# Performance work log

Measured on AMD Instinct MI355X. Metric: run time of the kernel, lower is better.

The kernel has to match this reference:

```python
import jax, jax.numpy as jnp
import numpy as np

GAMMA = 1.0
BIG = 1e30  # finite stand-in for +inf to keep gradients NaN-free


def pairwise_sqdist(x, y):
    # x: [B, C, N], y: [B, C, M] -> [B, N, M] squared euclidean distances
    xx = jnp.sum(x * x, axis=1)                      # [B, N]
    yy = jnp.sum(y * y, axis=1)                      # [B, M]
    xy = jnp.einsum('bcn,bcm->bnm', x, y)            # [B, N, M]
    return xx[:, :, None] + yy[:, None, :] - 2.0 * xy


def soft_dtw(D, gamma):
    # Anti-diagonal wavefront soft-DTW DP.
    # R[i, j] = D[i-1, j-1] + softmin(R[i-1,j-1], R[i-1,j], R[i,j-1])
    # Diagonal d = i + j; store diag as [B, N+1] arrays indexed by i.
    B, N, M = D.shape
    i_idx = jnp.arange(N + 1)
    # d = 0 diagonal: R[0,0] = 0, everything else +inf
    diag0 = jnp.full((B, N + 1), BIG, D.dtype).at[:, 0].set(0.0)
    # d = 1 diagonal: R[1,0] and R[0,1] are +inf
    diag1 = jnp.full((B, N + 1), BIG, D.dtype)

    def step(carry, d):
        prev2, prev1 = carry                      # diagonals d-2, d-1
        j = d - i_idx                             # 1-based column index
        valid = (i_idx >= 1) & (i_idx <= N) & (j >= 1) & (j <= M)
        di = jnp.clip(i_idx - 1, 0, N - 1)
        dj = jnp.clip(j - 1, 0, M - 1)
        dvals = D[:, di, dj]                      # [B, N+1]
        r0 = jnp.roll(prev2, 1, axis=1)           # R[i-1, j-1]
        r1 = jnp.roll(prev1, 1, axis=1)           # R[i-1, j]
        r2 = prev1                                # R[i, j-1]
        stacked = jnp.stack([r0, r1, r2], axis=0)  # [3, B, N+1]
        softmin = -gamma * jax.nn.logsumexp(-stacked / gamma, axis=0)
        cur = jnp.where(valid[None, :], dvals + softmin, BIG)
        return (prev1, cur), None

    ds = jnp.arange(2, N + M + 1)
    (_, last), _ = jax.lax.scan(step, (diag0, diag1), ds)
    return last[:, N]                             # R[N, M] per batch


def setup_inputs() -> dict:
    key = jax.random.key(0)
    kx, ky = jax.random.split(key)
    B, C, N = 32, 80, 512
    x = jax.random.normal(kx, (B, C, N), dtype=jnp.float32)
    y = jax.random.normal(ky, (B, C, N), dtype=jnp.float32)
    return {"x": x, "y": y}


def reference(x, y):
    D = pairwise_sqdist(x, y)     # save_memory=True path
    return soft_dtw(D, GAMMA)     # [B], normalize=False; squeeze(0) is a no-op
```

## Files before the change

kernel.cpp:

```cpp
#include <hip/hip_runtime.h>
#include <hip/hip_bf16.h>

#define BIGF 1e30f
#define TC 80
#define TN 512
#define L2E 1.4426950408889634f
#define LN2 0.6931471805599453f

typedef float f32x2 __attribute__((ext_vector_type(2)));
typedef float f32x4 __attribute__((ext_vector_type(4)));
typedef short s16x8 __attribute__((ext_vector_type(8)));
typedef __attribute__((address_space(1))) const unsigned int gu32;
typedef __attribute__((address_space(3))) unsigned int lu32;

__global__ __launch_bounds__(256) void pairdist_kernel(
    const float* __restrict__ x, const float* __restrict__ y,
    float* __restrict__ F) {
  const int b  = blockIdx.z;
  const int n0 = blockIdx.x * 128;
  const int m0 = blockIdx.y * 128;

  __shared__ __align__(16) short Ab[128 * 128];
  __shared__ __align__(16) short Bb[128 * 128];
  __shared__ float xxs[128], yys[128];

  const float* xb = x + (size_t)b * TC * TN;
  const float* yb = y + (size_t)b * TC * TN;
  const int tid = threadIdx.x;

  auto sw = [](int row, int k) -> int {
    return (row * 256 + k * 2) ^ ((row & 7) << 4);
  };
  auto cvt = [](float f) -> unsigned short {
    unsigned u = __float_as_uint(f);
    return (unsigned short)((u + 0x7FFFu + ((u >> 16) & 1u)) >> 16);
  };

  for (int item = tid; item < 12 * 128 * 2; item += 256) {
    int arr = (item >= 12 * 128) ? 1 : 0;
    int it  = item - arr * 12 * 128;
    int oct = it >> 7, n = it & 127;
    const float* src = arr ? (yb + m0 + n) : (xb + n0 + n);
    s16x8 pk;
#pragma unroll
    for (int j = 0; j < 8; ++j) {
      int c = oct * 8 + j;
      float v = (c < TC) ? src[(size_t)c * TN] : 0.f;
      pk[j] = (short)cvt(v);
    }
    short* dst = arr ? Bb : Ab;
    *(s16x8*)((char*)dst + sw(n, oct * 8)) = pk;
  }

  if (tid < 128) {
    float s = 0.f;
    for (int c = 0; c < TC; ++c) {
      float v = xb[(size_t)c * TN + n0 + tid];
      s += v * v;
    }
    xxs[tid] = s;
  } else {
    int n = tid - 128;
    float s = 0.f;
    for (int c = 0; c < TC; ++c) {
      float v = yb[(size_t)c * TN + m0 + n];
      s += v * v;
    }
    yys[n] = s;
  }
  __syncthreads();

  const int l  = tid & 63;
  const int w  = tid >> 6;
  const int wm = (w >> 1) * 64, wn = (w & 1) * 64;
  const int fr = l & 15;
  const int fk = (l >> 4) * 8;

  f32x4 acc[4][4] = {};
#pragma unroll
  for (int ks = 0; ks < 3; ++ks) {
    const int k0 = ks * 32 + fk;
    s16x8 af[4], bfr[4];
#pragma unroll
    for (int ta = 0; ta < 4; ++ta)
      af[ta] = *(const s16x8*)((const char*)Ab + sw(wm + ta * 16 + fr, k0));
#pragma unroll
    for (int tq = 0; tq < 4; ++tq)
      bfr[tq] = *(const s16x8*)((const char*)Bb + sw(wn + tq * 16 + fr, k0));
#pragma unroll
    for (int ta = 0; ta < 4; ++ta)
#pragma unroll
      for (int tq = 0; tq < 4; ++tq)
        acc[ta][tq] = __builtin_amdgcn_mfma_f32_16x16x32_bf16(
            af[ta], bfr[tq], acc[ta][tq], 0, 0, 0);
  }

  float* Fb = F + (size_t)b * TN * TN;
#pragma unroll
  for (int ta = 0; ta < 4; ++ta) {
    const int mb = wm + ta * 16 + (l >> 4) * 4;
#pragma unroll
    for (int r = 0; r < 4; ++r) {
      const int jj = n0 + mb + r;
      const float xxv = xxs[mb + r];
#pragma unroll
      for (int tq = 0; tq < 4; ++tq) {
        const int nn = wn + tq * 16 + fr;
        const int i  = m0 + nn;
        float val = (xxv + yys[nn] - 2.f * acc[ta][tq][r]) * L2E;
        int p = (jj + (i >> 1)) & (TN - 1);
        Fb[(size_t)p * TN + i] = val;
      }
    }
  }
}

__global__ __launch_bounds__(256) __attribute__((amdgpu_waves_per_eu(1)))
void sdtw_kernel(const float* __restrict__ Ft, float* __restrict__ out) {
  const int b   = blockIdx.x;
  const int tid = threadIdx.x;
  const int g   = tid & 63;
  const int w   = tid >> 6;
  const float* Fb = Ft + (size_t)b * TN * TN;

  __shared__ float ring[4][16][128];
  __shared__ f32x4 hand[3][2][4];

  if (tid < 24) {
    f32x4 iv; iv[0] = BIGF; iv[1] = BIGF; iv[2] = BIGF; iv[3] = BIGF;
    ((f32x4*)hand)[tid] = iv;
  }
  __syncthreads();

  float p0 = BIGF, p1 = BIGF;
  float up_p = (tid == 0) ? 0.f : BIGF;

  auto stage = [&](int slot, int u) {
    const float* gp =
        Fb + (size_t)((u - 15 * w) & (TN - 1)) * TN + w * 128 + g;
    __builtin_amdgcn_global_load_lds((gu32*)gp,        (lu32*)&ring[w][slot][0],  4, 0, 0);
    __builtin_amdgcn_global_load_lds((gu32*)(gp + 64), (lu32*)&ring[w][slot][64], 4, 0, 0);
  };

  const unsigned rbase =
      (unsigned)(size_t)(__attribute__((address_space(3))) float*)&ring[w][0][0];
  const unsigned hbase =
      (unsigned)(size_t)(__attribute__((address_space(3))) f32x4*)&hand[0][0][0];

  auto cell = [&](float d, float r0, float r1, float r2) -> float {
    float mn, md, mx;
    asm("v_min3_f32 %0, %3, %4, %5\n\t"
        "v_med3_f32 %1, %3, %4, %5\n\t"
        "v_max3_f32 %2, %3, %4, %5"
        : "=&v"(mn), "=&v"(md), "=&v"(mx)
        : "v"(r0), "v"(r1), "v"(r2));
    float e1 = __builtin_amdgcn_exp2f(mn - md);
    float e2 = __builtin_amdgcn_exp2f(mn - mx);
    float dm = d + mn;
    float ss = (1.0f + e1) + e2;
    return dm - __builtin_amdgcn_logf(ss);
  };

  auto body = [&](f32x2 d, float pubk) -> float {
    float upc = __int_as_float(__builtin_amdgcn_update_dpp(
        __float_as_int(pubk), __float_as_int(p1), 0x138, 0xf, 0xf, false));
    float c0 = cell(d[0], up_p, upc, p0);
    float c1 = cell(d[1], p0, c0, p1);
    p0 = c0; p1 = c1; up_p = upc;
    return c1;
  };

#pragma unroll
  for (int sl = 0; sl < 16; ++sl) stage(sl, sl);

  f32x2 d0, d1, d2, d3, d4, d5, d6, d7;
  f32x2 d8, d9, d10, d11, d12, d13, d14, d15;

  int s = 0;
  for (int B = 0; B < 50; ++B, s += 16) {
    __builtin_amdgcn_s_barrier();
    asm volatile("s_waitcnt vmcnt(0)" ::: "memory");

    unsigned ad = rbase + (unsigned)(g * 8);
    asm volatile(
        "ds_read_b64 %0, %16\n\t"
        "ds_read_b64 %1, %16 offset:512\n\t"
        "ds_read_b64 %2, %16 offset:1024\n\t"
        "ds_read_b64 %3, %16 offset:1536\n\t"
        "ds_read_b64 %4, %16 offset:2048\n\t"
        "ds_read_b64 %5, %16 offset:2560\n\t"
        "ds_read_b64 %6, %16 offset:3072\n\t"
        "ds_read_b64 %7, %16 offset:3584\n\t"
        "ds_read_b64 %8, %16 offset:4096\n\t"
        "ds_read_b64 %9, %16 offset:4608\n\t"
        "ds_read_b64 %10, %16 offset:5120\n\t"
        "ds_read_b64 %11, %16 offset:5632\n\t"
        "ds_read_b64 %12, %16 offset:6144\n\t"
        "ds_read_b64 %13, %16 offset:6656\n\t"
        "ds_read_b64 %14, %16 offset:7168\n\t"
        "ds_read_b64 %15, %16 offset:7680\n\t"
        "s_waitcnt lgkmcnt(0)"
        : "=&v"(d0), "=&v"(d1), "=&v"(d2), "=&v"(d3),
          "=&v"(d4), "=&v"(d5), "=&v"(d6), "=&v"(d7),
          "=&v"(d8), "=&v"(d9), "=&v"(d10), "=&v"(d11),
          "=&v"(d12), "=&v"(d13), "=&v"(d14), "=&v"(d15)
        : "v"(ad)
        : "memory");

    f32x4 pA, pB, pC, pD;
    if (w > 0) {
      unsigned ha = hbase + (unsigned)(((w - 1) * 2 + ((B + 1) & 1)) * 64);
      asm volatile("ds_read_b128 %0, %4\n\t"
                   "ds_read_b128 %1, %4 offset:16\n\t"
                   "ds_read_b128 %2, %4 offset:32\n\t"
                   "ds_read_b128 %3, %4 offset:48\n\t"
                   "s_waitcnt lgkmcnt(0)"
                   : "=&v"(pA), "=&v"(pB), "=&v"(pC), "=&v"(pD)
                   : "v"(ha) : "memory");
    } else {
      pA[0] = pA[1] = pA[2] = pA[3] = BIGF;
      pB[0] = pB[1] = pB[2] = pB[3] = BIGF;
      pC[0] = pC[1] = pC[2] = pC[3] = BIGF;
      pD[0] = pD[1] = pD[2] = pD[3] = BIGF;
    }

#pragma unroll
    for (int sl = 0; sl < 16; ++sl) stage(sl, s + 16 + sl);

    f32x4 k0, k1, k2, k3;
    k0[0] = body(d0, pA[0]);  k0[1] = body(d1, pA[1]);
    k0[2] = body(d2, pA[2]);  k0[3] = body(d3, pA[3]);
    k1[0] = body(d4, pB[0]);  k1[1] = body(d5, pB[1]);
    k1[2] = body(d6, pB[2]);  k1[3] = body(d7, pB[3]);
    k2[0] = body(d8, pC[0]);  k2[1] = body(d9, pC[1]);
    k2[2] = body(d10, pC[2]); k2[3] = body(d11, pC[3]);
    k3[0] = body(d12, pD[0]); k3[1] = body(d13, pD[1]);
    k3[2] = body(d14, pD[2]); k3[3] = body(d15, pD[3]);

    if (w < 3 && g == 63) {
      unsigned wa = hbase + (unsigned)((w * 2 + (B & 1)) * 64);
      asm volatile("ds_write_b128 %0, %1\n\t"
                   "ds_write_b128 %0, %2 offset:16\n\t"
                   "ds_write_b128 %0, %3 offset:32\n\t"
                   "ds_write_b128 %0, %4 offset:48\n\t"
                   "s_waitcnt lgkmcnt(0)"
                   :: "v"(wa), "v"(k0), "v"(k1), "v"(k2), "v"(k3)
                   : "memory");
    }
  }

  __builtin_amdgcn_s_barrier();
  asm volatile("s_waitcnt vmcnt(0)" ::: "memory");
  {
    unsigned ad = rbase + (unsigned)(g * 8);
    asm volatile(
        "ds_read_b64 %0, %12\n\t"
        "ds_read_b64 %1, %12 offset:512\n\t"
        "ds_read_b64 %2, %12 offset:1024\n\t"
        "ds_read_b64 %3, %12 offset:1536\n\t"
        "ds_read_b64 %4, %12 offset:2048\n\t"
        "ds_read_b64 %5, %12 offset:2560\n\t"
        "ds_read_b64 %6, %12 offset:3072\n\t"
        "ds_read_b64 %7, %12 offset:3584\n\t"
        "ds_read_b64 %8, %12 offset:4096\n\t"
        "ds_read_b64 %9, %12 offset:4608\n\t"
        "ds_read_b64 %10, %12 offset:5120\n\t"
        "ds_read_b64 %11, %12 offset:5632\n\t"
        "s_waitcnt lgkmcnt(0)"
        : "=&v"(d0), "=&v"(d1), "=&v"(d2), "=&v"(d3),
          "=&v"(d4), "=&v"(d5), "=&v"(d6), "=&v"(d7),
          "=&v"(d8), "=&v"(d9), "=&v"(d10), "=&v"(d11)
        : "v"(ad)
        : "memory");
  }
  f32x4 pA, pB, pC;
  if (w > 0) {
    unsigned ha = hbase + (unsigned)(((w - 1) * 2 + 1) * 64);
    asm volatile("ds_read_b128 %0, %3\n\t"
                 "ds_read_b128 %1, %3 offset:16\n\t"
                 "ds_read_b128 %2, %3 offset:32\n\t"
                 "s_waitcnt lgkmcnt(0)"
                 : "=&v"(pA), "=&v"(pB), "=&v"(pC) : "v"(ha) : "memory");
  } else {
    pA[0] = pA[1] = pA[2] = pA[3] = BIGF;
    pB[0] = pB[1] = pB[2] = pB[3] = BIGF;
    pC[0] = pC[1] = pC[2] = pC[3] = BIGF;
  }
  body(d0, pA[0]);  body(d1, pA[1]);  body(d2, pA[2]);  body(d3, pA[3]);
  body(d4, pB[0]);  body(d5, pB[1]);  body(d6, pB[2]);  body(d7, pB[3]);
  body(d8, pC[0]);  body(d9, pC[1]);  body(d10, pC[2]); body(d11, pC[3]);

  if (w == 3 && g == 63) out[b] = p1 * LN2;
}

extern "C" void kernel_launch(void* const* d_in, const int* in_sizes, int n_in,
                              void* d_out, int out_size, void* d_ws, size_t ws_size,
                              hipStream_t stream) {
  const float* x = (const float*)d_in[0];
  const float* y = (const float*)d_in[1];
  float* out = (float*)d_out;
  float* F = (float*)d_ws;

  dim3 g1(TN / 128, TN / 128, 32);
  pairdist_kernel<<<g1, 256, 0, stream>>>(y, x, F);
  sdtw_kernel<<<32, 256, 0, stream>>>(F, out);
}
```

Measured before the change: 172.5 us.

## Double superstep length in soft-DTW wavefront and switch to 16-byte LDS staging loads

Each barrier-separated superstep now processes 32 anti-diagonal pairs instead of 16. This halves the number of workgroup barriers and inter-wave handoff exchanges, and the LDS ring and handoff buffers double to match. Global-to-LDS staging now uses 16-byte global_load_lds transfers with half-wave row splitting instead of two 4-byte loads per row, and the staging issue is split across the two halves of each superstep. The costs are more LDS, a longer pipeline skew between waves (31 instead of 15) and a reworked tail with different step counts.

```diff
diff --git a/kernel.cpp b/kernel.cpp
--- a/kernel.cpp
+++ b/kernel.cpp
@@ -123,10 +123,10 @@
   const int w   = tid >> 6;
   const float* Fb = Ft + (size_t)b * TN * TN;
 
-  __shared__ float ring[4][16][128];
-  __shared__ f32x4 hand[3][2][4];
-
-  if (tid < 24) {
+  __shared__ float ring[4][32][128];
+  __shared__ f32x4 hand[3][2][8];
+
+  if (tid < 48) {
     f32x4 iv; iv[0] = BIGF; iv[1] = BIGF; iv[2] = BIGF; iv[3] = BIGF;
     ((f32x4*)hand)[tid] = iv;
   }
@@ -135,11 +135,12 @@
   float p0 = BIGF, p1 = BIGF;
   float up_p = (tid == 0) ? 0.f : BIGF;
 
-  auto stage = [&](int slot, int u) {
+  auto stage2 = [&](int k, int u0) {
+    int u = u0 + (g >> 5);
     const float* gp =
-        Fb + (size_t)((u - 15 * w) & (TN - 1)) * TN + w * 128 + g;
-    __builtin_amdgcn_global_load_lds((gu32*)gp,        (lu32*)&ring[w][slot][0],  4, 0, 0);
-    __builtin_amdgcn_global_load_lds((gu32*)(gp + 64), (lu32*)&ring[w][slot][64], 4, 0, 0);
+        Fb + (size_t)((u - 31 * w) & (TN - 1)) * TN + w * 128 + (g & 31) * 4;
+    __builtin_amdgcn_global_load_lds((gu32*)gp, (lu32*)&ring[w][k * 2][0],
+                                     16, 0, 0);
   };
 
   const unsigned rbase =
@@ -170,18 +171,10 @@
     return c1;
   };
 
-#pragma unroll
-  for (int sl = 0; sl < 16; ++sl) stage(sl, sl);
-
   f32x2 d0, d1, d2, d3, d4, d5, d6, d7;
   f32x2 d8, d9, d10, d11, d12, d13, d14, d15;
-
-  int s = 0;
-  for (int B = 0; B < 50; ++B, s += 16) {
-    __builtin_amdgcn_s_barrier();
-    asm volatile("s_waitcnt vmcnt(0)" ::: "memory");
-
-    unsigned ad = rbase + (unsigned)(g * 8);
+  auto read16 = [&](int base16) {
+    unsigned ad = rbase + (unsigned)(base16 * 8192) + (unsigned)(g * 8);
     asm volatile(
         "ds_read_b64 %0, %16\n\t"
         "ds_read_b64 %1, %16 offset:512\n\t"
@@ -206,53 +199,112 @@
           "=&v"(d12), "=&v"(d13), "=&v"(d14), "=&v"(d15)
         : "v"(ad)
         : "memory");
-
-    f32x4 pA, pB, pC, pD;
+  };
+
+#pragma unroll
+  for (int k = 0; k < 16; ++k) stage2(k, 2 * k);
+
+  int s = 0;
+  for (int B = 0; B < 26; ++B, s += 32) {
+    __builtin_amdgcn_s_barrier();
+    asm volatile("s_waitcnt vmcnt(0)" ::: "memory");
+
+    f32x4 m0, m1, m2, m3, m4, m5, m6, m7;
     if (w > 0) {
-      unsigned ha = hbase + (unsigned)(((w - 1) * 2 + ((B + 1) & 1)) * 64);
-      asm volatile("ds_read_b128 %0, %4\n\t"
-                   "ds_read_b128 %1, %4 offset:16\n\t"
-                   "ds_read_b128 %2, %4 offset:32\n\t"
-                   "ds_read_b128 %3, %4 offset:48\n\t"
+      unsigned ha = hbase + (unsigned)(((w - 1) * 2 + ((B + 1) & 1)) * 128);
+      asm volatile("ds_read_b128 %0, %8\n\t"
+                   "ds_read_b128 %1, %8 offset:16\n\t"
+                   "ds_read_b128 %2, %8 offset:32\n\t"
+                   "ds_read_b128 %3, %8 offset:48\n\t"
+                   "ds_read_b128 %4, %8 offset:64\n\t"
+                   "ds_read_b128 %5, %8 offset:80\n\t"
+                   "ds_read_b128 %6, %8 offset:96\n\t"
+                   "ds_read_b128 %7, %8 offset:112\n\t"
                    "s_waitcnt lgkmcnt(0)"
-                   : "=&v"(pA), "=&v"(pB), "=&v"(pC), "=&v"(pD)
+                   : "=&v"(m0), "=&v"(m1), "=&v"(m2), "=&v"(m3),
+                     "=&v"(m4), "=&v"(m5), "=&v"(m6), "=&v"(m7)
                    : "v"(ha) : "memory");
     } else {
-      pA[0] = pA[1] = pA[2] = pA[3] = BIGF;
-      pB[0] = pB[1] = pB[2] = pB[3] = BIGF;
-      pC[0] = pC[1] = pC[2] = pC[3] = BIGF;
-      pD[0] = pD[1] = pD[2] = pD[3] = BIGF;
-    }
-
-#pragma unroll
-    for (int sl = 0; sl < 16; ++sl) stage(sl, s + 16 + sl);
-
-    f32x4 k0, k1, k2, k3;
-    k0[0] = body(d0, pA[0]);  k0[1] = body(d1, pA[1]);
-    k0[2] = body(d2, pA[2]);  k0[3] = body(d3, pA[3]);
-    k1[0] = body(d4, pB[0]);  k1[1] = body(d5, pB[1]);
-    k1[2] = body(d6, pB[2]);  k1[3] = body(d7, pB[3]);
-    k2[0] = body(d8, pC[0]);  k2[1] = body(d9, pC[1]);
-    k2[2] = body(d10, pC[2]); k2[3] = body(d11, pC[3]);
-    k3[0] = body(d12, pD[0]); k3[1] = body(d13, pD[1]);
-    k3[2] = body(d14, pD[2]); k3[3] = body(d15, pD[3]);
+      m0[0]=m0[1]=m0[2]=m0[3]=BIGF; m1[0]=m1[1]=m1[2]=m1[3]=BIGF;
+      m2[0]=m2[1]=m2[2]=m2[3]=BIGF; m3[0]=m3[1]=m3[2]=m3[3]=BIGF;
+      m4[0]=m4[1]=m4[2]=m4[3]=BIGF; m5[0]=m5[1]=m5[2]=m5[3]=BIGF;
+      m6[0]=m6[1]=m6[2]=m6[3]=BIGF; m7[0]=m7[1]=m7[2]=m7[3]=BIGF;
+    }
+
+    f32x4 k0, k1, k2, k3, k4, k5, k6, k7;
+
+    read16(0);
+#pragma unroll
+    for (int k = 0; k < 8; ++k) stage2(k, s + 32 + 2 * k);
+    k0[0] = body(d0, m0[0]);  k0[1] = body(d1, m0[1]);
+    k0[2] = body(d2, m0[2]);  k0[3] = body(d3, m0[3]);
+    k1[0] = body(d4, m1[0]);  k1[1] = body(d5, m1[1]);
+    k1[2] = body(d6, m1[2]);  k1[3] = body(d7, m1[3]);
+    k2[0] = body(d8, m2[0]);  k2[1] = body(d9, m2[1]);
+    k2[2] = body(d10, m2[2]); k2[3] = body(d11, m2[3]);
+    k3[0] = body(d12, m3[0]); k3[1] = body(d13, m3[1]);
+    k3[2] = body(d14, m3[2]); k3[3] = body(d15, m3[3]);
+
+    read16(1);
+#pragma unroll
+    for (int k = 8; k < 16; ++k) stage2(k, s + 32 + 2 * k);
+    k4[0] = body(d0, m4[0]);  k4[1] = body(d1, m4[1]);
+    k4[2] = body(d2, m4[2]);  k4[3] = body(d3, m4[3]);
+    k5[0] = body(d4, m5[0]);  k5[1] = body(d5, m5[1]);
+    k5[2] = body(d6, m5[2]);  k5[3] = body(d7, m5[3]);
+    k6[0] = body(d8, m6[0]);  k6[1] = body(d9, m6[1]);
+    k6[2] = body(d10, m6[2]); k6[3] = body(d11, m6[3]);
+    k7[0] = body(d12, m7[0]); k7[1] = body(d13, m7[1]);
+    k7[2] = body(d14, m7[2]); k7[3] = body(d15, m7[3]);
 
     if (w < 3 && g == 63) {
-      unsigned wa = hbase + (unsigned)((w * 2 + (B & 1)) * 64);
+      unsigned wa = hbase + (unsigned)((w * 2 + (B & 1)) * 128);
       asm volatile("ds_write_b128 %0, %1\n\t"
                    "ds_write_b128 %0, %2 offset:16\n\t"
                    "ds_write_b128 %0, %3 offset:32\n\t"
                    "ds_write_b128 %0, %4 offset:48\n\t"
+                   "ds_write_b128 %0, %5 offset:64\n\t"
+                   "ds_write_b128 %0, %6 offset:80\n\t"
+                   "ds_write_b128 %0, %7 offset:96\n\t"
+                   "ds_write_b128 %0, %8 offset:112\n\t"
                    "s_waitcnt lgkmcnt(0)"
-                   :: "v"(wa), "v"(k0), "v"(k1), "v"(k2), "v"(k3)
+                   :: "v"(wa), "v"(k0), "v"(k1), "v"(k2), "v"(k3),
+                      "v"(k4), "v"(k5), "v"(k6), "v"(k7)
                    : "memory");
     }
   }
 
   __builtin_amdgcn_s_barrier();
   asm volatile("s_waitcnt vmcnt(0)" ::: "memory");
+  f32x4 m0, m1, m2, m3, m4, m5, m6;
+  if (w > 0) {
+    unsigned ha = hbase + (unsigned)(((w - 1) * 2 + 1) * 128);
+    asm volatile("ds_read_b128 %0, %7\n\t"
+                 "ds_read_b128 %1, %7 offset:16\n\t"
+                 "ds_read_b128 %2, %7 offset:32\n\t"
+                 "ds_read_b128 %3, %7 offset:48\n\t"
+                 "ds_read_b128 %4, %7 offset:64\n\t"
+                 "ds_read_b128 %5, %7 offset:80\n\t"
+                 "ds_read_b128 %6, %7 offset:96\n\t"
+                 "s_waitcnt lgkmcnt(0)"
+                 : "=&v"(m0), "=&v"(m1), "=&v"(m2), "=&v"(m3),
+                   "=&v"(m4), "=&v"(m5), "=&v"(m6)
+                 : "v"(ha) : "memory");
+  } else {
+    m0[0]=m0[1]=m0[2]=m0[3]=BIGF; m1[0]=m1[1]=m1[2]=m1[3]=BIGF;
+    m2[0]=m2[1]=m2[2]=m2[3]=BIGF; m3[0]=m3[1]=m3[2]=m3[3]=BIGF;
+    m4[0]=m4[1]=m4[2]=m4[3]=BIGF; m5[0]=m5[1]=m5[2]=m5[3]=BIGF;
+    m6[0]=m6[1]=m6[2]=m6[3]=BIGF;
+  }
+
+  read16(0);
+  body(d0, m0[0]);  body(d1, m0[1]);  body(d2, m0[2]);  body(d3, m0[3]);
+  body(d4, m1[0]);  body(d5, m1[1]);  body(d6, m1[2]);  body(d7, m1[3]);
+  body(d8, m2[0]);  body(d9, m2[1]);  body(d10, m2[2]); body(d11, m2[3]);
+  body(d12, m3[0]); body(d13, m3[1]); body(d14, m3[2]); body(d15, m3[3]);
+
   {
-    unsigned ad = rbase + (unsigned)(g * 8);
+    unsigned ad = rbase + 8192u + (unsigned)(g * 8);
     asm volatile(
         "ds_read_b64 %0, %12\n\t"
         "ds_read_b64 %1, %12 offset:512\n\t"
@@ -273,22 +325,9 @@
         : "v"(ad)
         : "memory");
   }
-  f32x4 pA, pB, pC;
-  if (w > 0) {
-    unsigned ha = hbase + (unsigned)(((w - 1) * 2 + 1) * 64);
-    asm volatile("ds_read_b128 %0, %3\n\t"
-                 "ds_read_b128 %1, %3 offset:16\n\t"
-                 "ds_read_b128 %2, %3 offset:32\n\t"
-                 "s_waitcnt lgkmcnt(0)"
-                 : "=&v"(pA), "=&v"(pB), "=&v"(pC) : "v"(ha) : "memory");
-  } else {
-    pA[0] = pA[1] = pA[2] = pA[3] = BIGF;
-    pB[0] = pB[1] = pB[2] = pB[3] = BIGF;
-    pC[0] = pC[1] = pC[2] = pC[3] = BIGF;
-  }
-  body(d0, pA[0]);  body(d1, pA[1]);  body(d2, pA[2]);  body(d3, pA[3]);
-  body(d4, pB[0]);  body(d5, pB[1]);  body(d6, pB[2]);  body(d7, pB[3]);
-  body(d8, pC[0]);  body(d9, pC[1]);  body(d10, pC[2]); body(d11, pC[3]);
+  body(d0, m4[0]);  body(d1, m4[1]);  body(d2, m4[2]);  body(d3, m4[3]);
+  body(d4, m5[0]);  body(d5, m5[1]);  body(d6, m5[2]);  body(d7, m5[3]);
+  body(d8, m6[0]);  body(d9, m6[1]);  body(d10, m6[2]); body(d11, m6[3]);
 
   if (w == 3 && g == 63) out[b] = p1 * LN2;
 }
```

New measurement: 158.3 us. 8.2% less time.
